# Performance work log

Measured on AMD Instinct MI355X. Metric: run time of the kernel, lower is better.

The kernel has to match this reference:

```python
import jax, jax.numpy as jnp
import numpy as np

# TT embedding config
IN_SHAPE = (100, 100, 100)      # vocab = 1_000_000
OUT_SHAPE = (4, 8, 4)           # embed_dim = 128
RANKS = (1, 32, 32, 32, 16, 8, 1)
OUT_SIZE = int(np.prod(OUT_SHAPE))
VOCAB = int(np.prod(IN_SHAPE))

def _xavier(key, shape):
    fan_in, fan_out = shape[0] * shape[1], shape[1] * shape[2]
    a = float(np.sqrt(6.0 / (shape[0] * shape[1] * shape[2] / shape[1] + 0)))  # placeholder
    # torch xavier_uniform on (r0, n, r1): fan_in = n*r1? torch treats dim0 as fan_out-ish;
    # exact init scale does not affect correctness checking, use a simple uniform bound.
    bound = float(np.sqrt(6.0 / (shape[0] * shape[1] + shape[1] * shape[2])))
    return jax.random.uniform(key, shape, jnp.float32, -bound, bound)

def setup_inputs() -> dict:
    key = jax.random.key(0)
    ks = jax.random.split(key, 7)
    idx = jax.random.randint(ks[0], (512, 128), 0, VOCAB, dtype=jnp.int32)
    shapes = [(RANKS[i], s, RANKS[i + 1]) for i, s in enumerate(IN_SHAPE + OUT_SHAPE)]
    cores = [_xavier(ks[i + 1], shapes[i]) for i in range(6)]
    return {"idx": idx, "core0": cores[0], "core1": cores[1], "core2": cores[2],
            "core3": cores[3], "core4": cores[4], "core5": cores[5]}

def reference(idx, core0, core1, core2, core3, core4, core5):
    in_shape = idx.shape
    flat = idx.reshape(-1)  # [N]
    # index decomposition with tt_index_factor = [10000, 100]
    i0 = flat // 10000
    i1 = (flat % 10000) // 100
    i2 = flat % 100
    # per-index gather + chained small batched matmuls over input cores
    g = core0[0, i0, :]                              # [N, r1]
    g = jnp.einsum('nr,rns->ns', g, core1[:, i1, :])  # [N, r2]
    g = jnp.einsum('nr,rns->ns', g, core2[:, i2, :])  # [N, r3]
    # contract output cores into a single [r3, OUT_SIZE] matrix (shared across batch)
    t = core3.reshape(-1, core4.shape[0]) @ core4.reshape(core4.shape[0], -1)
    t = t.reshape(-1, core5.shape[0]) @ core5.reshape(core5.shape[0], -1)
    W = t.reshape(RANKS[3], OUT_SIZE)                # [r3, 128]
    out = g @ W                                      # [N, 128]
    return out.reshape(in_shape + (OUT_SIZE,))
```

## Files before the change

### kernel.cpp

```cpp
#include <hip/hip_runtime.h>

#define N_TOKENS   65536
#define TOKS_PER_BLK 128
#define MAIN_TILES (N_TOKENS / TOKS_PER_BLK + 100)
#define ORD_SIZE    (MAIN_TILES * TOKS_PER_BLK)
#define NB_M2   100
#define NB_G1T  1250
#define NB_HIST 64
#define PREP_BLOCKS (NB_M2 + NB_G1T + NB_HIST)

#define WS_M2T  0
#define WS_G1T  204800
#define WS_CNT  364800
#define WS_ORD  372992
#define WS_NEED ((size_t)(372992 + ORD_SIZE) * 4)

typedef __attribute__((ext_vector_type(8))) short bf16x8;
typedef __attribute__((ext_vector_type(4))) float f32x4;

__device__ __forceinline__ unsigned short f2bf(float x) {
    union { float f; unsigned u; } v; v.f = x;
    unsigned r = v.u + 0x7FFF + ((v.u >> 16) & 1);
    return (unsigned short)(r >> 16);
}

__global__ __launch_bounds__(256) void prep(
    const int* __restrict__ idx,
    const float* __restrict__ c0, const float* __restrict__ c1,
    const float* __restrict__ c2, const float* __restrict__ c3,
    const float* __restrict__ c4, const float* __restrict__ c5,
    unsigned short* __restrict__ M2T, unsigned short* __restrict__ G1Tb,
    int* __restrict__ cnt) {
    __shared__ float smem[8768];
    const int b = blockIdx.x, t = threadIdx.x;

    if (b < NB_M2) {
        const int i2 = b;
        float* c4l = smem;
        float* c5l = smem + 1024;
        float* t45 = smem + 1056;
        float* c3l = smem + 1568;
        float* Wl  = smem + 3616;
        float* c2l = smem + 7712;
        *(float4*)(c4l + t * 4) = *(const float4*)(c4 + t * 4);
        if (t < 8) *(float4*)(c5l + t * 4) = *(const float4*)(c5 + t * 4);
        *(float4*)(c3l + t * 8)     = *(const float4*)(c3 + t * 8);
        *(float4*)(c3l + t * 8 + 4) = *(const float4*)(c3 + t * 8 + 4);
        {
            const int r = t >> 3, s4 = (t & 7) * 4;
            const float4 v = *(const float4*)(c2 + r * 3200 + i2 * 32 + s4);
            c2l[r * 33 + s4 + 0] = v.x;
            c2l[r * 33 + s4 + 1] = v.y;
            c2l[r * 33 + s4 + 2] = v.z;
            c2l[r * 33 + s4 + 3] = v.w;
        }
        __syncthreads();
#pragma unroll
        for (int k = 0; k < 2; ++k) {
            const int e = t + k * 256;
            const int q = e >> 5, u = e & 31;
            const int m1 = u >> 2, v = u & 3;
            float acc = 0.f;
#pragma unroll
            for (int m2 = 0; m2 < 8; ++m2)
                acc = fmaf(c4l[q * 64 + m1 * 8 + m2], c5l[m2 * 4 + v], acc);
            t45[e] = acc;
        }
        __syncthreads();
#pragma unroll 4
        for (int k = 0; k < 16; ++k) {
            const int e = t + k * 256;
            const int r = e >> 7, j = e & 127;
            const int p = j >> 5, u = j & 31;
            const float* c3row = c3l + (r * 4 + p) * 16;
            float acc = 0.f;
#pragma unroll
            for (int q = 0; q < 16; ++q)
                acc = fmaf(c3row[q], t45[q * 32 + u], acc);
            Wl[e] = acc;
        }
        __syncthreads();
#pragma unroll 4
        for (int k = 0; k < 16; ++k) {
            const int e = t + k * 256;
            const int j = e >> 5, r = e & 31;
            float acc = 0.f;
#pragma unroll
            for (int s = 0; s < 32; ++s)
                acc = fmaf(c2l[r * 33 + s], Wl[s * 128 + j], acc);
            M2T[i2 * 4096 + e] = f2bf(acc);
        }
    } else if (b < NB_M2 + NB_G1T) {
        const int pair = (b - NB_M2) * 8 + (t >> 5);
        const int s = t & 31;
        const int i0 = pair / 100;
        const int i1 = pair - i0 * 100;
        const float4* a4 = (const float4*)(c0 + i0 * 32);
        const float* c1p = c1 + i1 * 32 + s;
        float acc = 0.f;
#pragma unroll
        for (int r4 = 0; r4 < 8; ++r4) {
            const float4 a = a4[r4];
            acc = fmaf(a.x, c1p[(r4 * 4 + 0) * 3200], acc);
            acc = fmaf(a.y, c1p[(r4 * 4 + 1) * 3200], acc);
            acc = fmaf(a.z, c1p[(r4 * 4 + 2) * 3200], acc);
            acc = fmaf(a.w, c1p[(r4 * 4 + 3) * 3200], acc);
        }
        G1Tb[pair * 32 + s] = f2bf(acc);
    } else {
        const int hb = b - (NB_M2 + NB_G1T);
        int* lh = (int*)smem;
        if (t < 128) lh[t] = 0;
        __syncthreads();
#pragma unroll
        for (int k = 0; k < 4; ++k) {
            const int n = hb * 1024 + k * 256 + t;
            atomicAdd(&lh[idx[n] % 100], 1);
        }
        __syncthreads();
        if (t < 128) cnt[hb * 128 + t] = lh[t];
    }
}

__global__ __launch_bounds__(256) void sort2(const int* __restrict__ idx,
                                             const int* __restrict__ cnt,
                                             int* __restrict__ order) {
    __shared__ int cm[64 * 128];
    __shared__ int totals[100];
    __shared__ int offsj[100];
    __shared__ int sb[101];
    __shared__ int lhj[100];
    const int j = blockIdx.x, t = threadIdx.x;
    {
        const int4* src = (const int4*)cnt;
        int4* dst = (int4*)cm;
#pragma unroll
        for (int k = 0; k < 8; ++k) dst[t + k * 256] = src[t + k * 256];
    }
    if (t < 100) lhj[t] = 0;
    __syncthreads();
    if (t < 100) {
        int tot = 0, off = 0;
        for (int hb = 0; hb < 64; ++hb) {
            const int c = cm[hb * 128 + t];
            if (hb < j) off += c;
            tot += c;
        }
        totals[t] = tot;
        offsj[t] = off;
    }
    __syncthreads();
    if (t < 64) {
        const int e0 = 2 * t, e1 = 2 * t + 1;
        const int p0 = (e0 < 100) ? ((totals[e0] + 127) & ~127) : 0;
        const int p1 = (e1 < 100) ? ((totals[e1] + 127) & ~127) : 0;
        const int pair = p0 + p1;
        int incl = pair;
#pragma unroll
        for (int d = 1; d < 64; d <<= 1) {
            const int v = __shfl_up(incl, d, 64);
            if (t >= d) incl += v;
        }
        const int base = incl - pair;
        if (e0 < 100) sb[e0] = base;
        if (e1 < 100) sb[e1] = base + p0;
        if (t == 63) sb[100] = incl;
    }
    __syncthreads();
    int bkt[4], rnk[4];
#pragma unroll
    for (int k = 0; k < 4; ++k) {
        const int n = j * 1024 + k * 256 + t;
        const int bb = idx[n] % 100;
        bkt[k] = bb;
        rnk[k] = atomicAdd(&lhj[bb], 1);
    }
#pragma unroll
    for (int k = 0; k < 4; ++k) {
        const int n = j * 1024 + k * 256 + t;
        order[sb[bkt[k]] + offsj[bkt[k]] + rnk[k]] = n;
    }
    for (int bb = j; bb < 100; bb += 64) {
        const int tot = totals[bb];
        const int pt = (tot + 127) & ~127;
        for (int i = tot + t; i < pt; i += 256) order[sb[bb] + i] = -1;
    }
    {
        const int gt = sb[100];
        for (int i = gt + j * 256 + t; i < ORD_SIZE; i += 64 * 256) order[i] = -1;
    }
}

__global__ __launch_bounds__(256) void tt_main(
    const int* __restrict__ idx, const int* __restrict__ order,
    const unsigned short* __restrict__ G1Tb, const unsigned short* __restrict__ M2T,
    float* __restrict__ out) {
    __shared__ unsigned short g1b[128 * 40];
    __shared__ unsigned short m2t[128 * 40];
    __shared__ int toks[TOKS_PER_BLK];

    const int t = threadIdx.x;
    const int base = blockIdx.x * TOKS_PER_BLK;
    const int n0 = order[base];
    if (n0 < 0) return;
    const int i2v = idx[n0] % 100;

    {
        const int tk = t >> 1, half = t & 1;
        const int n = order[base + tk];
        int4 v0 = {0, 0, 0, 0}, v1 = {0, 0, 0, 0};
        if (n >= 0) {
            const int pair = idx[n] / 100;
            const int4* g = (const int4*)(G1Tb + pair * 32);
            v0 = g[half * 2];
            v1 = g[half * 2 + 1];
        }
        int4* d = (int4*)(g1b + tk * 40 + half * 16);
        d[0] = v0;
        d[1] = v1;
        if (t < TOKS_PER_BLK) toks[t] = order[base + t];
    }
    {
        const int j = t >> 1, half = t & 1;
        const int4* s = (const int4*)(M2T + i2v * 4096 + j * 32);
        int4* d = (int4*)(m2t + j * 40 + half * 16);
        d[0] = s[half * 2];
        d[1] = s[half * 2 + 1];
    }
    __syncthreads();

    const int wid  = t >> 6;
    const int lane = t & 63;
    const int ln15 = lane & 15;
    const int q8   = (lane >> 4) * 8;

    f32x4 acc[2][8];
#pragma unroll
    for (int a = 0; a < 2; ++a)
#pragma unroll
        for (int c = 0; c < 8; ++c) acc[a][c] = (f32x4){0.f, 0.f, 0.f, 0.f};

    bf16x8 af[2], bf[8];
#pragma unroll
    for (int trr = 0; trr < 2; ++trr) {
        const int tok = (2 * wid + trr) * 16 + ln15;
        af[trr] = *(const bf16x8*)(g1b + tok * 40 + q8);
    }
#pragma unroll
    for (int tc = 0; tc < 8; ++tc) {
        const int j = tc * 16 + ln15;
        bf[tc] = *(const bf16x8*)(m2t + j * 40 + q8);
    }
#pragma unroll
    for (int trr = 0; trr < 2; ++trr)
#pragma unroll
        for (int tc = 0; tc < 8; ++tc)
            acc[trr][tc] = __builtin_amdgcn_mfma_f32_16x16x32_bf16(
                af[trr], bf[tc], acc[trr][tc], 0, 0, 0);

    const int rowq = (lane >> 4) * 4;
#pragma unroll
    for (int trr = 0; trr < 2; ++trr) {
#pragma unroll
        for (int reg = 0; reg < 4; ++reg) {
            const int tokr = (2 * wid + trr) * 16 + rowq + reg;
            const int n = toks[tokr];
            if (n >= 0) {
                float* o = out + (size_t)n * 128 + ln15;
#pragma unroll
                for (int tc = 0; tc < 8; ++tc) o[tc * 16] = acc[trr][tc][reg];
            }
        }
    }
}

__global__ void build_w(const float* __restrict__ c3, const float* __restrict__ c4,
                        const float* __restrict__ c5, float* __restrict__ W) {
    int t = blockIdx.x * blockDim.x + threadIdx.x;
    if (t >= 32 * 128) return;
    int r = t >> 7;
    int j = t & 127;
    int p  = j >> 5;
    int m1 = (j >> 2) & 7;
    int v  = j & 3;
    const float* c3row = c3 + (r * 4 + p) * 16;
    float acc = 0.f;
#pragma unroll
    for (int m2 = 0; m2 < 8; ++m2) {
        float t1 = 0.f;
#pragma unroll
        for (int q = 0; q < 16; ++q)
            t1 += c3row[q] * c4[q * 64 + m1 * 8 + m2];
        acc += t1 * c5[m2 * 4 + v];
    }
    W[r * 128 + j] = acc;
}

__global__ __launch_bounds__(256, 4) void tt_embed_fb(
    const int* __restrict__ idx, const float* __restrict__ c0,
    const float* __restrict__ c1, const float* __restrict__ c2,
    const float* __restrict__ Wg, float* __restrict__ out) {
    __shared__ float Wl[32 * 128];
    __shared__ float g2l[8][32];
    const int t = threadIdx.x;
    {
        const float4* Wg4 = (const float4*)Wg;
        float4* Wl4 = (float4*)Wl;
#pragma unroll
        for (int i = 0; i < 4; ++i) Wl4[t + i * 256] = Wg4[t + i * 256];
    }
    __syncthreads();
    const int tt = t >> 5, s = t & 31;
    const int blockBase = blockIdx.x * 32;
    for (int round = 0; round < 4; ++round) {
        const int n = blockBase + round * 8 + tt;
        const int iv = idx[n];
        const int i0 = iv / 10000;
        const int rem = iv - i0 * 10000;
        const int i1 = rem / 100;
        const int i2 = rem - i1 * 100;
        const float4* c0r4 = (const float4*)(c0 + i0 * 32);
        const float* c1p = c1 + i1 * 32 + s;
        float g1 = 0.f;
#pragma unroll
        for (int r4 = 0; r4 < 8; ++r4) {
            float4 a = c0r4[r4];
            g1 += a.x * c1p[(r4 * 4 + 0) * 3200];
            g1 += a.y * c1p[(r4 * 4 + 1) * 3200];
            g1 += a.z * c1p[(r4 * 4 + 2) * 3200];
            g1 += a.w * c1p[(r4 * 4 + 3) * 3200];
        }
        const float* c2p = c2 + i2 * 32 + s;
        float g2 = 0.f;
#pragma unroll
        for (int r = 0; r < 32; ++r) {
            float g1r = __shfl(g1, r, 32);
            g2 += g1r * c2p[r * 3200];
        }
        g2l[tt][s] = g2;
        __syncthreads();
        float4 acc = {0.f, 0.f, 0.f, 0.f};
        const float4* Wl4 = (const float4*)Wl;
#pragma unroll
        for (int r = 0; r < 32; ++r) {
            const float g = g2l[tt][r];
            const float4 w = Wl4[r * 32 + s];
            acc.x += g * w.x; acc.y += g * w.y; acc.z += g * w.z; acc.w += g * w.w;
        }
        float4* outp = (float4*)(out + (size_t)n * 128);
        outp[s] = acc;
        __syncthreads();
    }
}

extern "C" void kernel_launch(void* const* d_in, const int* in_sizes, int n_in,
                              void* d_out, int out_size, void* d_ws, size_t ws_size,
                              hipStream_t stream) {
    const int*   idx = (const int*)d_in[0];
    const float* c0  = (const float*)d_in[1];
    const float* c1  = (const float*)d_in[2];
    const float* c2  = (const float*)d_in[3];
    const float* c3  = (const float*)d_in[4];
    const float* c4  = (const float*)d_in[5];
    const float* c5  = (const float*)d_in[6];
    float* out = (float*)d_out;
    float* ws  = (float*)d_ws;

    if (ws_size >= WS_NEED) {
        unsigned short* M2T  = (unsigned short*)(ws + WS_M2T);
        unsigned short* G1Tb = (unsigned short*)(ws + WS_G1T);
        int* cnt   = (int*)(ws + WS_CNT);
        int* order = (int*)(ws + WS_ORD);

        hipLaunchKernelGGL(prep,  dim3(PREP_BLOCKS), dim3(256), 0, stream,
                           idx, c0, c1, c2, c3, c4, c5, M2T, G1Tb, cnt);
        hipLaunchKernelGGL(sort2, dim3(NB_HIST), dim3(256), 0, stream, idx, cnt, order);
        hipLaunchKernelGGL(tt_main, dim3(MAIN_TILES), dim3(256), 0, stream,
                           idx, order, G1Tb, M2T, out);
    } else {
        float* W = ws;
        hipLaunchKernelGGL(build_w, dim3(16), dim3(256), 0, stream, c3, c4, c5, W);
        hipLaunchKernelGGL(tt_embed_fb, dim3(N_TOKENS / 32), dim3(256), 0, stream,
                           idx, c0, c1, c2, W, out);
    }
}
```

Measured before the change: 30.05 us.

## Fold histogram and sort into prep kernel, each sort block recomputing full histogram

Removes the separate sort2 launch and the global count buffer. Each of the 64 sort blocks now rebuilds the full 64x100 histogram from all 65536 indices in shared memory, then computes offsets and scatters its own chunk. These blocks run alongside the M2T and G1T precompute blocks in one launch. This saves one kernel launch and its dependency gap, at the cost of each sort block reading all of idx and doing many more shared-memory atomics.

```diff
diff --git a/kernel.cpp b/kernel.cpp
--- a/kernel.cpp
+++ b/kernel.cpp
@@ -4,16 +4,15 @@
 #define TOKS_PER_BLK 128
 #define MAIN_TILES (N_TOKENS / TOKS_PER_BLK + 100)
 #define ORD_SIZE    (MAIN_TILES * TOKS_PER_BLK)
+#define NB_SORT 64
 #define NB_M2   100
 #define NB_G1T  1250
-#define NB_HIST 64
-#define PREP_BLOCKS (NB_M2 + NB_G1T + NB_HIST)
+#define PREP2_BLOCKS (NB_SORT + NB_M2 + NB_G1T)
 
 #define WS_M2T  0
 #define WS_G1T  204800
-#define WS_CNT  364800
-#define WS_ORD  372992
-#define WS_NEED ((size_t)(372992 + ORD_SIZE) * 4)
+#define WS_ORD  364800
+#define WS_NEED ((size_t)(364800 + ORD_SIZE) * 4)
 
 typedef __attribute__((ext_vector_type(8))) short bf16x8;
 typedef __attribute__((ext_vector_type(4))) float f32x4;
@@ -24,18 +23,90 @@
     return (unsigned short)(r >> 16);
 }
 
-__global__ __launch_bounds__(256) void prep(
+__global__ __launch_bounds__(256) void prep2(
     const int* __restrict__ idx,
     const float* __restrict__ c0, const float* __restrict__ c1,
     const float* __restrict__ c2, const float* __restrict__ c3,
     const float* __restrict__ c4, const float* __restrict__ c5,
     unsigned short* __restrict__ M2T, unsigned short* __restrict__ G1Tb,
-    int* __restrict__ cnt) {
+    int* __restrict__ order) {
     __shared__ float smem[8768];
     const int b = blockIdx.x, t = threadIdx.x;
 
-    if (b < NB_M2) {
-        const int i2 = b;
+    if (b < NB_SORT) {
+        const int j = b;
+        int* cm     = (int*)smem;
+        int* totals = cm + 6400;
+        int* offsj  = totals + 100;
+        int* sb     = offsj + 100;
+        int* lhj    = sb + 101;
+        for (int i = t; i < 6400; i += 256) cm[i] = 0;
+        if (t < 100) lhj[t] = 0;
+        __syncthreads();
+        {
+            const int4* idx4 = (const int4*)idx;
+            for (int i = t; i < N_TOKENS / 4; i += 256) {
+                const int4 v = idx4[i];
+                int* row = cm + (i >> 8) * 100;
+                atomicAdd(&row[v.x % 100], 1);
+                atomicAdd(&row[v.y % 100], 1);
+                atomicAdd(&row[v.z % 100], 1);
+                atomicAdd(&row[v.w % 100], 1);
+            }
+        }
+        __syncthreads();
+        if (t < 100) {
+            int tot = 0, off = 0;
+            for (int hb = 0; hb < 64; ++hb) {
+                const int c = cm[hb * 100 + t];
+                if (hb < j) off += c;
+                tot += c;
+            }
+            totals[t] = tot;
+            offsj[t] = off;
+        }
+        __syncthreads();
+        if (t < 64) {
+            const int e0 = 2 * t, e1 = 2 * t + 1;
+            const int p0 = (e0 < 100) ? ((totals[e0] + 127) & ~127) : 0;
+            const int p1 = (e1 < 100) ? ((totals[e1] + 127) & ~127) : 0;
+            const int pair = p0 + p1;
+            int incl = pair;
+#pragma unroll
+            for (int d = 1; d < 64; d <<= 1) {
+                const int v = __shfl_up(incl, d, 64);
+                if (t >= d) incl += v;
+            }
+            const int base = incl - pair;
+            if (e0 < 100) sb[e0] = base;
+            if (e1 < 100) sb[e1] = base + p0;
+            if (t == 63) sb[100] = incl;
+        }
+        __syncthreads();
+        int bkt[4], rnk[4];
+#pragma unroll
+        for (int k = 0; k < 4; ++k) {
+            const int n = j * 1024 + k * 256 + t;
+            const int bb = idx[n] % 100;
+            bkt[k] = bb;
+            rnk[k] = atomicAdd(&lhj[bb], 1);
+        }
+#pragma unroll
+        for (int k = 0; k < 4; ++k) {
+            const int n = j * 1024 + k * 256 + t;
+            order[sb[bkt[k]] + offsj[bkt[k]] + rnk[k]] = n;
+        }
+        for (int bb = j; bb < 100; bb += 64) {
+            const int tot = totals[bb];
+            const int pt = (tot + 127) & ~127;
+            for (int i = tot + t; i < pt; i += 256) order[sb[bb] + i] = -1;
+        }
+        {
+            const int gt = sb[100];
+            for (int i = gt + j * 256 + t; i < ORD_SIZE; i += 64 * 256) order[i] = -1;
+        }
+    } else if (b < NB_SORT + NB_M2) {
+        const int i2 = b - NB_SORT;
         float* c4l = smem;
         float* c5l = smem + 1024;
         float* t45 = smem + 1056;
@@ -70,8 +141,8 @@
 #pragma unroll 4
         for (int k = 0; k < 16; ++k) {
             const int e = t + k * 256;
-            const int r = e >> 7, j = e & 127;
-            const int p = j >> 5, u = j & 31;
+            const int r = e >> 7, jj = e & 127;
+            const int p = jj >> 5, u = jj & 31;
             const float* c3row = c3l + (r * 4 + p) * 16;
             float acc = 0.f;
 #pragma unroll
@@ -83,15 +154,15 @@
 #pragma unroll 4
         for (int k = 0; k < 16; ++k) {
             const int e = t + k * 256;
-            const int j = e >> 5, r = e & 31;
+            const int jj = e >> 5, r = e & 31;
             float acc = 0.f;
 #pragma unroll
             for (int s = 0; s < 32; ++s)
-                acc = fmaf(c2l[r * 33 + s], Wl[s * 128 + j], acc);
+                acc = fmaf(c2l[r * 33 + s], Wl[s * 128 + jj], acc);
             M2T[i2 * 4096 + e] = f2bf(acc);
         }
-    } else if (b < NB_M2 + NB_G1T) {
-        const int pair = (b - NB_M2) * 8 + (t >> 5);
+    } else {
+        const int pair = (b - NB_SORT - NB_M2) * 8 + (t >> 5);
         const int s = t & 31;
         const int i0 = pair / 100;
         const int i1 = pair - i0 * 100;
@@ -107,87 +178,6 @@
             acc = fmaf(a.w, c1p[(r4 * 4 + 3) * 3200], acc);
         }
         G1Tb[pair * 32 + s] = f2bf(acc);
-    } else {
-        const int hb = b - (NB_M2 + NB_G1T);
-        int* lh = (int*)smem;
-        if (t < 128) lh[t] = 0;
-        __syncthreads();
-#pragma unroll
-        for (int k = 0; k < 4; ++k) {
-            const int n = hb * 1024 + k * 256 + t;
-            atomicAdd(&lh[idx[n] % 100], 1);
-        }
-        __syncthreads();
-        if (t < 128) cnt[hb * 128 + t] = lh[t];
-    }
-}
-
-__global__ __launch_bounds__(256) void sort2(const int* __restrict__ idx,
-                                             const int* __restrict__ cnt,
-                                             int* __restrict__ order) {
-    __shared__ int cm[64 * 128];
-    __shared__ int totals[100];
-    __shared__ int offsj[100];
-    __shared__ int sb[101];
-    __shared__ int lhj[100];
-    const int j = blockIdx.x, t = threadIdx.x;
-    {
-        const int4* src = (const int4*)cnt;
-        int4* dst = (int4*)cm;
-#pragma unroll
-        for (int k = 0; k < 8; ++k) dst[t + k * 256] = src[t + k * 256];
-    }
-    if (t < 100) lhj[t] = 0;
-    __syncthreads();
-    if (t < 100) {
-        int tot = 0, off = 0;
-        for (int hb = 0; hb < 64; ++hb) {
-            const int c = cm[hb * 128 + t];
-            if (hb < j) off += c;
-            tot += c;
-        }
-        totals[t] = tot;
-        offsj[t] = off;
-    }
-    __syncthreads();
-    if (t < 64) {
-        const int e0 = 2 * t, e1 = 2 * t + 1;
-        const int p0 = (e0 < 100) ? ((totals[e0] + 127) & ~127) : 0;
-        const int p1 = (e1 < 100) ? ((totals[e1] + 127) & ~127) : 0;
-        const int pair = p0 + p1;
-        int incl = pair;
-#pragma unroll
-        for (int d = 1; d < 64; d <<= 1) {
-            const int v = __shfl_up(incl, d, 64);
-            if (t >= d) incl += v;
-        }
-        const int base = incl - pair;
-        if (e0 < 100) sb[e0] = base;
-        if (e1 < 100) sb[e1] = base + p0;
-        if (t == 63) sb[100] = incl;
-    }
-    __syncthreads();
-    int bkt[4], rnk[4];
-#pragma unroll
-    for (int k = 0; k < 4; ++k) {
-        const int n = j * 1024 + k * 256 + t;
-        const int bb = idx[n] % 100;
-        bkt[k] = bb;
-        rnk[k] = atomicAdd(&lhj[bb], 1);
-    }
-#pragma unroll
-    for (int k = 0; k < 4; ++k) {
-        const int n = j * 1024 + k * 256 + t;
-        order[sb[bkt[k]] + offsj[bkt[k]] + rnk[k]] = n;
-    }
-    for (int bb = j; bb < 100; bb += 64) {
-        const int tot = totals[bb];
-        const int pt = (tot + 127) & ~127;
-        for (int i = tot + t; i < pt; i += 256) order[sb[bb] + i] = -1;
-    }
-    {
-        const int gt = sb[100];
-        for (int i = gt + j * 256 + t; i < ORD_SIZE; i += 64 * 256) order[i] = -1;
     }
 }
 
@@ -240,7 +230,7 @@
 #pragma unroll
         for (int c = 0; c < 8; ++c) acc[a][c] = (f32x4){0.f, 0.f, 0.f, 0.f};
 
-    bf16x8 af[2], bf[8];
+    bf16x8 af[2], bfr[8];
 #pragma unroll
     for (int trr = 0; trr < 2; ++trr) {
         const int tok = (2 * wid + trr) * 16 + ln15;
@@ -249,14 +239,14 @@
 #pragma unroll
     for (int tc = 0; tc < 8; ++tc) {
         const int j = tc * 16 + ln15;
-        bf[tc] = *(const bf16x8*)(m2t + j * 40 + q8);
+        bfr[tc] = *(const bf16x8*)(m2t + j * 40 + q8);
     }
 #pragma unroll
     for (int trr = 0; trr < 2; ++trr)
 #pragma unroll
         for (int tc = 0; tc < 8; ++tc)
             acc[trr][tc] = __builtin_amdgcn_mfma_f32_16x16x32_bf16(
-                af[trr], bf[tc], acc[trr][tc], 0, 0, 0);
+                af[trr], bfr[tc], acc[trr][tc], 0, 0, 0);
 
     const int rowq = (lane >> 4) * 4;
 #pragma unroll
@@ -369,12 +359,10 @@
     if (ws_size >= WS_NEED) {
         unsigned short* M2T  = (unsigned short*)(ws + WS_M2T);
         unsigned short* G1Tb = (unsigned short*)(ws + WS_G1T);
-        int* cnt   = (int*)(ws + WS_CNT);
         int* order = (int*)(ws + WS_ORD);
 
-        hipLaunchKernelGGL(prep,  dim3(PREP_BLOCKS), dim3(256), 0, stream,
-                           idx, c0, c1, c2, c3, c4, c5, M2T, G1Tb, cnt);
-        hipLaunchKernelGGL(sort2, dim3(NB_HIST), dim3(256), 0, stream, idx, cnt, order);
+        hipLaunchKernelGGL(prep2, dim3(PREP2_BLOCKS), dim3(256), 0, stream,
+                           idx, c0, c1, c2, c3, c4, c5, M2T, G1Tb, order);
         hipLaunchKernelGGL(tt_main, dim3(MAIN_TILES), dim3(256), 0, stream,
                            idx, order, G1Tb, M2T, out);
     } else {
```

Result: slower. 40.07 us (+33.3%).
